# Performance work log

Measured on AMD Instinct MI355X. Metric: run time of the kernel, lower is better.

## Reference

```python
import jax, jax.numpy as jnp
import numpy as np

S, B, L = 64, 32, 64
VS, VT = 32000, 32000
D_EMB, H_ENC, H_DEC = 300, 512, 1024


def _lstm_cell(x, h, c, w_ih, w_hh, b):
    # PyTorch gate order: i, f, g, o
    g = x @ w_ih.T + h @ w_hh.T + b
    i, f, gg, o = jnp.split(g, 4, axis=1)
    c2 = jax.nn.sigmoid(f) * c + jax.nn.sigmoid(i) * jnp.tanh(gg)
    h2 = jax.nn.sigmoid(o) * jnp.tanh(c2)
    return h2, c2


def _lstm_dir(emb, w_ih, w_hh, b, reverse):
    h0 = jnp.zeros((emb.shape[1], H_ENC), emb.dtype)
    def step(carry, x):
        h, c = carry
        h, c = _lstm_cell(x, h, c, w_ih, w_hh, b)
        return (h, c), h
    (hT, cT), ys = jax.lax.scan(step, (h0, h0), emb, reverse=reverse)
    return ys, hT, cT


def setup_inputs() -> dict:
    key = jax.random.key(0)
    ks = jax.random.split(key, 20)
    r = lambda k, shape: (jax.random.normal(k, shape, jnp.float32) * 0.02)
    inp = {
        "eemb": r(ks[0], (VS, D_EMB)),
        "enc_w_ih_f": r(ks[1], (4 * H_ENC, D_EMB)),
        "enc_w_hh_f": r(ks[2], (4 * H_ENC, H_ENC)),
        "enc_b_f": r(ks[3], (4 * H_ENC,)),  # = b_ih + b_hh (summed, identical math)
        "enc_w_ih_b": r(ks[4], (4 * H_ENC, D_EMB)),
        "enc_w_hh_b": r(ks[5], (4 * H_ENC, H_ENC)),
        "enc_b_b": r(ks[6], (4 * H_ENC,)),
        "attn_wi": r(ks[7], (H_DEC, H_DEC)),
        "attn_wo": r(ks[8], (H_DEC, 2 * H_DEC)),
        "dec_w_ih": r(ks[9], (4 * H_DEC, H_DEC + D_EMB)),
        "dec_w_hh": r(ks[10], (4 * H_DEC, H_DEC)),
        "dec_b": r(ks[11], (4 * H_DEC,)),
        "demb": r(ks[12], (VT, D_EMB)),
        "gen_w": r(ks[13], (VT, H_DEC)),
        "gen_b": r(ks[14], (VT,)),
        "input_src_batch": jax.random.randint(ks[15], (S, B), 0, VS),
        "input_trg_batch": jax.random.randint(ks[16], (L, B), 0, VT),
    }
    return inp


def reference(eemb, enc_w_ih_f, enc_w_hh_f, enc_b_f, enc_w_ih_b, enc_w_hh_b,
              enc_b_b, attn_wi, attn_wo, dec_w_ih, dec_w_hh, dec_b, demb,
              gen_w, gen_b, input_src_batch, input_trg_batch):
    emb = eemb[input_src_batch]  # [S,B,300]
    out_f, hf, cf = _lstm_dir(emb, enc_w_ih_f, enc_w_hh_f, enc_b_f, False)
    out_b, hb, cb = _lstm_dir(emb, enc_w_ih_b, enc_w_hh_b, enc_b_b, True)
    enc_out = jnp.concatenate([out_f, out_b], axis=2)  # [S,B,1024]
    bsz = emb.shape[1]
    # permute(1,2,0).view(B,1024): interleave fwd/bwd features
    hidden = jnp.stack([hf, hb], 0).transpose(1, 2, 0).reshape(bsz, H_DEC)
    context = jnp.stack([cf, cb], 0).transpose(1, 2, 0).reshape(bsz, H_DEC)

    trg_emb = demb[input_trg_batch[:-1]]  # [L-1,B,300]

    def dec_step(carry, e):
        h, c = carry
        semi = h @ attn_wi.T  # [B,1024]
        scores = jax.nn.softmax(jnp.sum(enc_out * semi[None], axis=2), axis=0)  # [S,B]
        s_tilde = jnp.sum(scores[:, :, None] * enc_out, axis=0)  # [B,1024]
        c_t = jnp.tanh(jnp.concatenate([s_tilde, h], axis=1) @ attn_wo.T)
        x = jnp.concatenate([c_t, e], axis=1)  # [B,1324]
        h, c = _lstm_cell(x, h, c, dec_w_ih, dec_w_hh, dec_b)
        out = jax.nn.log_softmax(h @ gen_w.T + gen_b, axis=1)  # [B,VT]
        return (h, c), out

    _, ys = jax.lax.scan(dec_step, (hidden, context), trg_emb)  # [L-1,B,VT]
    output = jnp.concatenate([jnp.zeros((1,) + ys.shape[1:], ys.dtype), ys], axis=0)
    return output
```

## Files before the change

kernel.cpp:

```cpp
#include <hip/hip_runtime.h>

typedef __attribute__((ext_vector_type(8))) short short8;
typedef __attribute__((ext_vector_type(4))) float f32x4;
typedef unsigned short u16;
typedef unsigned int u32;

static __device__ __forceinline__ float sigf(float x){ return 1.0f/(1.0f+__expf(-x)); }
static __device__ __forceinline__ float ftanh(float x){
    float e = __expf(2.0f*x);
    return 1.0f - 2.0f/(e + 1.0f);
}

static __device__ __forceinline__ u16 f2b(float f){
    u32 u = __float_as_uint(f);
    u += 0x7FFFu + ((u>>16)&1u);
    return (u16)(u>>16);
}
static __device__ __forceinline__ float us2f(u16 s){ return __uint_as_float(((u32)s)<<16); }
static __device__ __forceinline__ float b2f_lo(u32 u){ return __uint_as_float(u<<16); }
static __device__ __forceinline__ float b2f_hi(u32 u){ return __uint_as_float(u & 0xffff0000u); }

static __device__ __forceinline__ void st_wt_u16(u16* p, u16 v) {
    asm volatile("global_store_short %0, %1, off sc1" :: "v"(p), "v"((u32)v) : "memory");
}
static __device__ __forceinline__ void st_wt_u32(u32* p, u32 v) {
    asm volatile("global_store_dword %0, %1, off sc1" :: "v"(p), "v"(v) : "memory");
}
static __device__ __forceinline__ u32 ld_cv(const u32* p){
    u32 v;
    asm volatile("global_load_dword %0, %1, off sc0 sc1\ns_waitcnt vmcnt(0)"
                 : "=v"(v) : "v"(p) : "memory");
    return v;
}

static __device__ __forceinline__ void hot_spin() {
    float x = 1.0f;
#pragma unroll
    for (int i = 0; i < 16; ++i) x = __builtin_fmaf(x, 1.0000001f, 1.0e-7f);
    asm volatile("" :: "v"(x));
}

static __device__ __forceinline__ void wait_publish(const u32* base, int n, u32 tgt, u32* rel) {
    if ((int)threadIdx.x < n) {
        const u32* p = base + (size_t)threadIdx.x*32;
        while (ld_cv(p) < tgt) hot_spin();
    }
    __syncthreads();
    if (threadIdx.x == 0) st_wt_u32(rel, tgt);
}
static __device__ __forceinline__ void wait_rel(const u32* rel, u32 tgt) {
    if (threadIdx.x == 0) {
        while (ld_cv(rel) < tgt) hot_spin();
    }
    __syncthreads();
}


__global__ __launch_bounds__(256) void k_zero(float* __restrict__ p, long n) {
    for (long i = (long)blockIdx.x*256 + threadIdx.x; i < n; i += (long)gridDim.x*256) p[i] = 0.0f;
}

__global__ __launch_bounds__(256) void k_wenc2(const float* __restrict__ whhf,
                                               const float* __restrict__ whhb,
                                               u16* __restrict__ dst) {
    long i = (long)blockIdx.x*256 + threadIdx.x;
    int half = (int)(i >> 20);
    int ii = (int)(i & 1048575);
    int n = ii >> 9, k = ii & 511;
    int j = n >> 2, q = n & 3;
    const float* w = half ? whhb : whhf;
    dst[i] = f2b(w[(size_t)(q*512 + j)*512 + k]);
}

__global__ __launch_bounds__(256) void k_xw(const float* __restrict__ table,
                                            const int* __restrict__ idx,
                                            const float* __restrict__ W,
                                            int wstride, int koff,
                                            const float* __restrict__ bias,
                                            u16* __restrict__ outU, int N,
                                            int jmask, int jshift) {
    __shared__ float Xs[32][300];
    int m0 = blockIdx.y * 32;
    int j0 = blockIdx.x * 64;
    for (int i = threadIdx.x; i < 32*300; i += 256) {
        int r = i/300, c = i - r*300;
        Xs[r][c] = table[(size_t)idx[m0+r]*300 + c];
    }
    __syncthreads();
    int tx = threadIdx.x & 63, ty = threadIdx.x >> 6;
    int jj = j0 + tx;
    const float* wr = W + (size_t)jj*wstride + koff;
    float acc[8] = {0,0,0,0,0,0,0,0};
    for (int k = 0; k < 300; ++k) {
        float w = wr[k];
#pragma unroll
        for (int mi = 0; mi < 8; ++mi) acc[mi] += Xs[ty*8+mi][k] * w;
    }
    float bv = bias[jj];
    int col = ((jj & jmask) << 2) | (jj >> jshift);
#pragma unroll
    for (int mi = 0; mi < 8; ++mi)
        outU[(size_t)(m0 + ty*8 + mi)*N + col] = f2b(acc[mi] + bv);
}

__global__ __launch_bounds__(512, 1) void k_enc(
    const u16* __restrict__ Xf, const u16* __restrict__ Xb,
    const u16* __restrict__ WencB,
    u16* __restrict__ encBX, float* __restrict__ cfin,
    u32* __restrict__ sentE, u32* __restrict__ relE,
    const float* __restrict__ awi, const float* __restrict__ awo,
    const float* __restrict__ dwih, const float* __restrict__ dwhh,
    const float* __restrict__ genw,
    u16* __restrict__ awiTB, u16* __restrict__ awoB,
    u16* __restrict__ WdecB, u16* __restrict__ genw_b)
{
    __shared__ float SH[2304];
    const int tid = threadIdx.x;
    const int bid = blockIdx.x;

    if (bid >= 64) {
        long wid = (long)(bid-64)*512 + tid;
        {
            const float4* s4 = (const float4*)genw;
            ushort4* d4 = (ushort4*)genw_b;
            for (long i = wid; i < 8192000L; i += 98304L) {
                float4 v = s4[i]; ushort4 u;
                u.x=f2b(v.x); u.y=f2b(v.y); u.z=f2b(v.z); u.w=f2b(v.w);
                d4[i]=u;
            }
        }
        for (long i = wid; i < 8388608L; i += 98304L) {
            int n=(int)(i>>11), k=(int)(i&2047);
            int j=n>>2, q=n&3;
            float v=(k<1024)? dwih[(size_t)(q*1024+j)*1324+k]
                            : dwhh[(size_t)(q*1024+j)*1024+(k-1024)];
            WdecB[i]=f2b(v);
        }
        for (long i = wid; i < 1048576L; i += 98304L) {
            int kcol=(int)(i>>10), n=(int)(i&1023);
            awiTB[i]=f2b(awi[(size_t)n*1024+kcol]);
        }
        {
            const float4* s4=(const float4*)awo;
            ushort4* d4=(ushort4*)awoB;
            for (long i = wid; i < 524288L; i += 98304L) {
                float4 v=s4[i]; ushort4 u;
                u.x=f2b(v.x); u.y=f2b(v.y); u.z=f2b(v.z); u.w=f2b(v.w);
                d4[i]=u;
            }
        }
        return;
    }

    const int wv = tid >> 6, lane = tid & 63;
    const int gwave = bid*8 + wv;
    const int lr = lane & 15, lk8 = (lane >> 4)*8;
    const int b_l = lane & 15, jjq = lane >> 4;
    const int g0 = bid & 48;
    u32* relg = relE + (size_t)(g0 >> 4)*32;

    const int dir = gwave >> 8;
    const int mt = (gwave >> 7) & 1;
    const int nt = gwave & 127;
    const int m0 = mt*16, n0 = nt*16;
    const u16* Bw = WencB + (size_t)dir*1048576 + (size_t)(n0+lr)*512 + lk8;
    const u16* Xd = dir ? Xb : Xf;
    float* T = SH + wv*272;
    const int bb = m0 + b_l;
    const int j = nt*4 + jjq;

    short8 bw[16];
#pragma unroll
    for (int i = 0; i < 16; ++i) bw[i] = *(const short8*)(Bw + i*32);

    float creg = 0.f;
    for (int t = 0; t < 64; ++t) {
        if (t > 0) {
            if (bid == g0) wait_publish(sentE + (size_t)g0*32, 16, (u32)t, relg);
            else           wait_rel(relg, (u32)t);
        }
        const int rslot = (t==0) ? 0 : (dir ? (65-t) : t);
        const u16* Ah = encBX + (size_t)rslot*32768 + (size_t)(m0+lr)*1024 + dir*512 + lk8;
        short8 av[16];
#pragma unroll
        for (int i = 0; i < 16; ++i) av[i] = *(const short8*)(Ah + i*32);
        f32x4 acc = {0.f,0.f,0.f,0.f};
#pragma unroll
        for (int i = 0; i < 16; ++i)
            acc = __builtin_amdgcn_mfma_f32_16x16x32_bf16(av[i], bw[i], acc, 0, 0, 0);
        {
            const int rb = (lane>>4)*4;
#pragma unroll
            for (int r = 0; r < 4; ++r) T[(rb+r)*17 + (lane&15)] = acc[r];
        }
        __builtin_amdgcn_sched_barrier(0);
        const int s = dir ? (63-t) : t;
        ushort4 xr = *(const ushort4*)(Xd + (size_t)(s*32+bb)*2048 + n0 + jjq*4);
        float gi = T[b_l*17 + jjq*4 + 0] + us2f(xr.x);
        float gf = T[b_l*17 + jjq*4 + 1] + us2f(xr.y);
        float gg = T[b_l*17 + jjq*4 + 2] + us2f(xr.z);
        float go = T[b_l*17 + jjq*4 + 3] + us2f(xr.w);
        float c2 = sigf(gf)*creg + sigf(gi)*ftanh(gg);
        float h2 = sigf(go)*ftanh(c2);
        creg = c2;
        st_wt_u16(encBX + (size_t)(s+1)*32768 + (size_t)bb*1024 + dir*512 + j, f2b(h2));
        __syncthreads();
        if (tid == 0) st_wt_u32(sentE + (size_t)bid*32, (u32)(t+1));
    }
    cfin[dir*16384 + bb*512 + j] = creg;
}

__global__ __launch_bounds__(256) void k_mid(const u16* __restrict__ encBX,
                                             const u16* __restrict__ awiTB,
                                             const u16* __restrict__ awoB,
                                             u16* __restrict__ encPB,
                                             u16* __restrict__ EOAb,
                                             u16* __restrict__ Hd) {
    if (blockIdx.x < 128) {
        int gt = blockIdx.x*256 + threadIdx.x;
        int b = gt >> 10, jj2 = gt & 1023;
        int d = jj2 & 1, k = jj2 >> 1;
        Hd[(size_t)b*1024 + jj2] = encBX[(size_t)(d ? 1 : 64)*32768 + (size_t)b*1024 + d*512 + k];
        Hd[(size_t)64*32768 + gt] = 0;
    }
    const int wv = threadIdx.x >> 6, lane = threadIdx.x & 63;
    const int lr = lane & 15, lk8 = (lane >> 4)*8;
    const u16* Abase = encBX + 32768;
#pragma unroll
    for (int ii = 0; ii < 4; ++ii) {
        int id = (blockIdx.x*4 + wv)*4 + ii;
        int eoa = id >> 13;
        int id2 = id & 8191;
        int mt2 = id2 >> 6, nt2 = id2 & 63;
        int m0 = mt2*16, n0 = nt2*16;
        const u16* Ar = Abase + (size_t)(m0+lr)*1024 + lk8;
        const u16* Br = eoa ? (awoB + (size_t)(n0+lr)*2048 + lk8)
                            : (awiTB + (size_t)(n0+lr)*1024 + lk8);
        f32x4 acc = {0.f,0.f,0.f,0.f};
#pragma unroll 8
        for (int i = 0; i < 32; ++i) {
            short8 av = *(const short8*)(Ar + i*32);
            short8 bv = *(const short8*)(Br + i*32);
            acc = __builtin_amdgcn_mfma_f32_16x16x32_bf16(av, bv, acc, 0, 0, 0);
        }
        int col = n0 + (lane&15);
        int rb = m0 + (lane>>4)*4;
#pragma unroll
        for (int r = 0; r < 4; ++r) {
            int row = rb + r;
            if (eoa) {
                int b = row & 31, s = row >> 5;
                EOAb[((size_t)b*64 + s)*1024 + col] = f2b(acc[r]);
            } else {
                encPB[(size_t)row*1024 + col] = f2b(acc[r]);
            }
        }
    }
}

__global__ __launch_bounds__(512, 1) void k_dec(
    const u16* __restrict__ Xe,
    const u16* __restrict__ awoB, const u16* __restrict__ WdecB,
    const u16* __restrict__ encPB, const u16* __restrict__ EOAb,
    u16* __restrict__ Hd, u16* __restrict__ PEOb, u16* __restrict__ hAb,
    const float* __restrict__ cfin,
    u32* __restrict__ sentA, u32* __restrict__ sentH,
    u32* __restrict__ relA, u32* __restrict__ relH)
{
    __shared__ float SH[2592];
    __shared__ u32 CT[16512];
    const int tid = threadIdx.x;
    const int bid = blockIdx.x;
    const int wv = tid >> 6, lane = tid & 63;
    const int lr = lane & 15, lk8 = (lane >> 4)*8;
    const int b_l = lane & 15, jjq = lane >> 4;

    const int mt4 = wv & 1, kq4 = wv >> 1;
    const int m0d = mt4*16;
    const int bbd = m0d + b_l;
    const int jd = bid*4 + jjq;
    float cdec = cfin[(jd&1)*16384 + bbd*512 + (jd>>1)];

    short8 wp[16];
#pragma unroll
    for (int i = 0; i < 16; ++i)
        wp[i] = *(const short8*)(WdecB + (size_t)(bid*16+lr)*2048 + kq4*512 + lk8 + i*32);

    const bool isHA = (bid >= 32 && bid < 96);
    const int nth = bid - 32;
    const int mth = wv & 1, kqh = wv >> 1;
    short8 wh[8];
    if (isHA) {
#pragma unroll
        for (int i = 0; i < 8; ++i)
            wh[i] = *(const short8*)(awoB + (size_t)(nth*16+lr)*2048 + 1024 + kqh*256 + lk8 + i*32);
    }

    for (int t = 0; t < 63; ++t) {
        if (bid < 96) {
            if (t > 0) {
                if (bid == 0) wait_publish(sentH, 256, (u32)t, relH);
                else          wait_rel(relH, (u32)t);
            }
            if (bid < 32) {
                const int b = bid;
                float* hsh = SH; float* red = SH + 1024; float* sc = SH + 1536;
                {
                    u32 u = ((const u32*)Hd)[(size_t)t*16384 + b*512 + tid];
                    hsh[2*tid]   = b2f_lo(u);
                    hsh[2*tid+1] = b2f_hi(u);
                }
                __syncthreads();
                {
                    int s = tid >> 3, p = tid & 7;
                    const uint4* ep = (const uint4*)(encPB + (size_t)(s*32+b)*1024 + p*128);
                    const float* hk = hsh + p*128;
                    float a0=0,a1=0,a2=0,a3=0;
#pragma unroll 4
                    for (int q8 = 0; q8 < 16; ++q8) {
                        uint4 u = ep[q8];
                        a0 += b2f_lo(u.x)*hk[q8*8+0] + b2f_hi(u.x)*hk[q8*8+1];
                        a1 += b2f_lo(u.y)*hk[q8*8+2] + b2f_hi(u.y)*hk[q8*8+3];
                        a2 += b2f_lo(u.z)*hk[q8*8+4] + b2f_hi(u.z)*hk[q8*8+5];
                        a3 += b2f_lo(u.w)*hk[q8*8+6] + b2f_hi(u.w)*hk[q8*8+7];
                    }
                    red[tid] = (a0+a1)+(a2+a3);
                }
                __syncthreads();
                if (tid < 64) {
                    float v = 0;
#pragma unroll
                    for (int pp = 0; pp < 8; ++pp) v += red[tid*8+pp];
                    float m = v;
                    for (int off = 32; off; off >>= 1) m = fmaxf(m, __shfl_xor(m, off));
                    float e = __expf(v - m);
                    float ss = e;
                    for (int off = 32; off; off >>= 1) ss += __shfl_xor(ss, off);
                    sc[tid] = e / ss;
                }
                __syncthreads();
                {
                    const u32* eo = (const u32*)EOAb + (size_t)b*32768 + tid;
                    float p0 = 0, p1 = 0;
#pragma unroll 8
                    for (int s = 0; s < 64; ++s) {
                        u32 u = eo[(size_t)s*512];
                        float w = sc[s];
                        p0 += w*b2f_lo(u); p1 += w*b2f_hi(u);
                    }
                    u32 pk = (u32)f2b(p0) | ((u32)f2b(p1) << 16);
                    st_wt_u32((u32*)PEOb + (size_t)t*16384 + b*512 + tid, pk);
                }
            } else {
                const u16* Ah = Hd + (size_t)t*32768 + (size_t)(mth*16+lr)*1024 + kqh*256 + lk8;
                short8 av[8];
#pragma unroll
                for (int i = 0; i < 8; ++i) av[i] = *(const short8*)(Ah + i*32);
                f32x4 acc = {0.f,0.f,0.f,0.f};
#pragma unroll
                for (int i = 0; i < 8; ++i)
                    acc = __builtin_amdgcn_mfma_f32_16x16x32_bf16(av[i], wh[i], acc, 0, 0, 0);
#pragma unroll
                for (int r = 0; r < 4; ++r) SH[wv*256 + lane*4 + r] = acc[r];
                __syncthreads();
                if (wv < 2) {
#pragma unroll
                    for (int r = 0; r < 4; ++r) {
                        float sum = SH[(wv+0)*256 + lane*4 + r] + SH[(wv+2)*256 + lane*4 + r]
                                  + SH[(wv+4)*256 + lane*4 + r] + SH[(wv+6)*256 + lane*4 + r];
                        int m = wv*16 + (lane>>4)*4 + r;
                        st_wt_u16(hAb + (size_t)t*32768 + (size_t)m*1024 + nth*16 + (lane&15),
                                  f2b(sum));
                    }
                }
            }
            __syncthreads();
            if (tid == 0) st_wt_u32(sentA + (size_t)bid*32, (u32)(t+1));
        }

        if (bid == 96) wait_publish(sentA, 96, (u32)(t+1), relA);
        else           wait_rel(relA, (u32)(t+1));
        {
            const u32* pe = (const u32*)PEOb + (size_t)t*16384;
            const u32* ha = (const u32*)hAb + (size_t)t*16384;
#pragma unroll
            for (int ii = 0; ii < 32; ++ii) {
                int idx = tid + ii*512;
                u32 up = pe[idx], uh = ha[idx];
                float c0 = ftanh(b2f_lo(up) + b2f_lo(uh));
                float c1 = ftanh(b2f_hi(up) + b2f_hi(uh));
                int b = idx >> 9, nu = idx & 511;
                CT[b*516 + nu] = (u32)f2b(c0) | ((u32)f2b(c1) << 16);
            }
            __syncthreads();

            short8 av[16];
            if (kq4 < 2) {
                const u32* ctrow = CT + (m0d+lr)*516 + kq4*256 + (lk8 >> 1);
#pragma unroll
                for (int i = 0; i < 16; ++i) av[i] = *(const short8*)(ctrow + i*16);
            } else {
                const u16* Ab = Hd + (size_t)t*32768 + (size_t)(m0d+lr)*1024 + (kq4-2)*512 + lk8;
#pragma unroll
                for (int i = 0; i < 16; ++i) av[i] = *(const short8*)(Ab + i*32);
            }
            f32x4 acc = {0.f,0.f,0.f,0.f};
#pragma unroll
            for (int i = 0; i < 16; ++i)
                acc = __builtin_amdgcn_mfma_f32_16x16x32_bf16(av[i], wp[i], acc, 0, 0, 0);
#pragma unroll
            for (int r = 0; r < 4; ++r) SH[wv*256 + lane*4 + r] = acc[r];
            __syncthreads();
            if (wv < 2) {
                float* T = SH + 2048 + wv*272;
#pragma unroll
                for (int r = 0; r < 4; ++r) {
                    float sum = SH[(wv+0)*256 + lane*4 + r] + SH[(wv+2)*256 + lane*4 + r]
                              + SH[(wv+4)*256 + lane*4 + r] + SH[(wv+6)*256 + lane*4 + r];
                    T[((lane>>4)*4 + r)*17 + (lane&15)] = sum;
                }
                __builtin_amdgcn_sched_barrier(0);
                ushort4 xr = *(const ushort4*)(Xe + (size_t)(t*32+bbd)*4096 + bid*16 + jjq*4);
                float gi = T[b_l*17 + jjq*4 + 0] + us2f(xr.x);
                float gf = T[b_l*17 + jjq*4 + 1] + us2f(xr.y);
                float gg = T[b_l*17 + jjq*4 + 2] + us2f(xr.z);
                float go = T[b_l*17 + jjq*4 + 3] + us2f(xr.w);
                float c2 = sigf(gf)*cdec + sigf(gi)*ftanh(gg);
                float h2 = sigf(go)*ftanh(c2);
                cdec = c2;
                st_wt_u16(Hd + (size_t)(t+1)*32768 + (size_t)bbd*1024 + jd, f2b(h2));
            }
            __syncthreads();
            if (tid == 0) st_wt_u32(sentH + (size_t)bid*32, (u32)(t+1));
        }
    }
}

__global__ __launch_bounds__(256, 1) void k_gemm_gen(const short* __restrict__ A,
                                                     const short* __restrict__ B,
                                                     const float* __restrict__ genb,
                                                     float* __restrict__ out) {
    int wave = threadIdx.x >> 6;
    int lane = threadIdx.x & 63;
    int tile = blockIdx.x * 4 + wave;
    int mt = tile & 15;
    int nt = tile >> 4;
    int m0 = mt*128, n0 = nt*64;
    int lr = lane & 15;
    int lk = (lane >> 4)*8;
    f32x4 acc[8][4] = {};
    for (int k0 = 0; k0 < 1024; k0 += 32) {
        short8 bfr[4];
#pragma unroll
        for (int ni = 0; ni < 4; ++ni)
            bfr[ni] = *(const short8*)(B + (long)(n0 + ni*16 + lr)*1024 + k0 + lk);
#pragma unroll
        for (int mi = 0; mi < 8; ++mi) {
            short8 a = *(const short8*)(A + (long)(m0 + mi*16 + lr)*1024 + k0 + lk);
#pragma unroll
            for (int ni = 0; ni < 4; ++ni)
                acc[mi][ni] = __builtin_amdgcn_mfma_f32_16x16x32_bf16(a, bfr[ni], acc[mi][ni], 0, 0, 0);
        }
    }
    int dcol = lane & 15;
    int drow = (lane >> 4)*4;
#pragma unroll
    for (int mi = 0; mi < 8; ++mi) {
        int mbase = m0 + mi*16 + drow;
#pragma unroll
        for (int ni = 0; ni < 4; ++ni) {
            int n = n0 + ni*16 + dcol;
            float bv = genb[n];
            f32x4 v = acc[mi][ni];
#pragma unroll
            for (int r = 0; r < 4; ++r) {
                int m = mbase + r;
                if (m < 2016) out[(long)(m + 32)*32000 + n] = v[r] + bv;
            }
        }
    }
}

__global__ __launch_bounds__(256) void k_lsm(float* __restrict__ out) {
    long row = 32 + blockIdx.x;
    float* p = out + row*32000L;
    float4* p4 = (float4*)p;
    int tid = threadIdx.x;
    __shared__ float sm[4];
    __shared__ float ss[4];
    float m = -1e30f;
    for (int i = tid; i < 8000; i += 256) {
        float4 v = p4[i];
        m = fmaxf(m, fmaxf(fmaxf(v.x, v.y), fmaxf(v.z, v.w)));
    }
    for (int off = 32; off; off >>= 1) m = fmaxf(m, __shfl_xor(m, off));
    if ((tid & 63) == 0) sm[tid >> 6] = m;
    __syncthreads();
    m = fmaxf(fmaxf(sm[0], sm[1]), fmaxf(sm[2], sm[3]));
    float s = 0;
    for (int i = tid; i < 8000; i += 256) {
        float4 v = p4[i];
        s += __expf(v.x - m) + __expf(v.y - m) + __expf(v.z - m) + __expf(v.w - m);
    }
    for (int off = 32; off; off >>= 1) s += __shfl_xor(s, off);
    if ((tid & 63) == 0) ss[tid >> 6] = s;
    __syncthreads();
    s = ss[0] + ss[1] + ss[2] + ss[3];
    float lse = m + __logf(s);
    for (int i = tid; i < 8000; i += 256) {
        float4 v = p4[i];
        v.x -= lse; v.y -= lse; v.z -= lse; v.w -= lse;
        p4[i] = v;
    }
}


extern "C" void kernel_launch(void* const* d_in, const int* in_sizes, int n_in,
                              void* d_out, int out_size, void* d_ws, size_t ws_size,
                              hipStream_t stream) {
    const float* eemb  = (const float*)d_in[0];
    const float* ewihf = (const float*)d_in[1];
    const float* ewhhf = (const float*)d_in[2];
    const float* ebf   = (const float*)d_in[3];
    const float* ewihb = (const float*)d_in[4];
    const float* ewhhb = (const float*)d_in[5];
    const float* ebb   = (const float*)d_in[6];
    const float* awi   = (const float*)d_in[7];
    const float* awo   = (const float*)d_in[8];
    const float* dwih  = (const float*)d_in[9];
    const float* dwhh  = (const float*)d_in[10];
    const float* db    = (const float*)d_in[11];
    const float* demb  = (const float*)d_in[12];
    const float* genw  = (const float*)d_in[13];
    const float* genb  = (const float*)d_in[14];
    const int* srci    = (const int*)d_in[15];
    const int* trgi    = (const int*)d_in[16];
    float* out = (float*)d_out;

    float* F = (float*)d_ws;
    u32* S       = (u32*)F;
    u32* sentE   = S;
    u32* sentA   = S + 2048;
    u32* sentH   = S + 5120;
    u32* relE    = S + 13312;
    u32* relA    = S + 13440;
    u32* relH    = S + 13472;
    float* cfin  = F + 16384;
    u16*   U     = (u16*)(F + 49152);

    u16* Xf_    = U;
    u16* Xb_    = U + 4194304u;
    u16* Xe_    = U + 8388608u;
    u16* WencB  = U + 16646144u;
    u16* awiTB  = U + 18743296u;
    u16* awoB   = U + 19791872u;
    u16* WdecB  = U + 21889024u;
    u16* genw_b = U + 30277632u;
    u16* encBX  = U + 63045632u;
    u16* Hd     = U + 65175552u;
    u16* PEOb   = U + 67305472u;
    u16* hAb    = U + 69369856u;
    u16* encPB  = U + 71434240u;
    u16* EOAb   = U + 73531392u;

    k_zero<<<64, 256, 0, stream>>>(F, 16384);
    k_zero<<<64, 256, 0, stream>>>((float*)encBX, 16384);
    k_zero<<<2048, 256, 0, stream>>>(out, 1024000L);

    k_xw<<<dim3(32, 64), 256, 0, stream>>>(eemb, srci, ewihf, 300, 0, ebf, Xf_, 2048, 511, 9);
    k_xw<<<dim3(32, 64), 256, 0, stream>>>(eemb, srci, ewihb, 300, 0, ebb, Xb_, 2048, 511, 9);
    k_xw<<<dim3(64, 63), 256, 0, stream>>>(demb, trgi, dwih, 1324, 1024, db, Xe_, 4096, 1023, 10);

    k_wenc2<<<8192, 256, 0, stream>>>(ewhhf, ewhhb, WencB);

    k_enc<<<256, 512, 0, stream>>>(Xf_, Xb_, WencB, encBX, cfin, sentE, relE,
                                   awi, awo, dwih, dwhh, genw,
                                   awiTB, awoB, WdecB, genw_b);
    k_mid<<<1024, 256, 0, stream>>>(encBX, awiTB, awoB, encPB, EOAb, Hd);

    k_dec<<<256, 512, 0, stream>>>(Xe_, awoB, WdecB, encPB, EOAb,
                                   Hd, PEOb, hAb, cfin,
                                   sentA, sentH, relA, relH);

    k_gemm_gen<<<2000, 256, 0, stream>>>((const short*)(Hd + 32768u), (const short*)genw_b, genb, out);
    k_lsm<<<2016, 256, 0, stream>>>(out);
}
```

Baseline: 2.633 ms.

## Overlap generator GEMM with decoder recurrence inside persistent decode kernel

Halves the number of blocks doing the decoder LSTM update, so each block now handles two batch halves (32 gate columns), which frees blocks 128-255. Those freed blocks compute the vocabulary projection GEMM in chunks of 256 rows as soon as the corresponding hidden states are published. The aim is to hide the large generator GEMM behind the latency-bound sequential decode and drop a separate kernel launch. In exchange, the decoder blocks do twice the MFMA work per step, the shared-memory footprint grows, and the GEMM blocks compete with the recurrence for bandwidth and caches.

```diff
diff --git a/kernel.cpp b/kernel.cpp
--- a/kernel.cpp
+++ b/kernel.cpp
@@ -264,10 +264,11 @@
     const u16* __restrict__ encPB, const u16* __restrict__ EOAb,
     u16* __restrict__ Hd, u16* __restrict__ PEOb, u16* __restrict__ hAb,
     const float* __restrict__ cfin,
+    const u16* __restrict__ genw_b, const float* __restrict__ genb, float* __restrict__ out,
     u32* __restrict__ sentA, u32* __restrict__ sentH,
     u32* __restrict__ relA, u32* __restrict__ relH)
 {
-    __shared__ float SH[2592];
+    __shared__ float SH[5184];
     __shared__ u32 CT[16512];
     const int tid = threadIdx.x;
     const int bid = blockIdx.x;
@@ -275,16 +276,64 @@
     const int lr = lane & 15, lk8 = (lane >> 4)*8;
     const int b_l = lane & 15, jjq = lane >> 4;
 
-    const int mt4 = wv & 1, kq4 = wv >> 1;
-    const int m0d = mt4*16;
-    const int bbd = m0d + b_l;
-    const int jd = bid*4 + jjq;
-    float cdec = cfin[(jd&1)*16384 + bbd*512 + (jd>>1)];
+    if (bid >= 128) {
+        const int gw = (bid - 128)*8 + wv;
+        const u16* A = Hd + 32768;
+        for (int c = 0; c < 8; ++c) {
+            u32 need = (c == 7) ? 63u : (u32)(8*c + 8);
+            wait_rel(relH, need);
+            int tile = gw;
+            if (tile < 1000) {
+                int m0 = c*256 + (tile & 1)*128;
+                int n0 = (tile >> 1)*64;
+                f32x4 acc[8][4] = {};
+                for (int k0 = 0; k0 < 1024; k0 += 32) {
+                    short8 bfr[4];
+#pragma unroll
+                    for (int ni = 0; ni < 4; ++ni)
+                        bfr[ni] = *(const short8*)(genw_b + (size_t)(n0 + ni*16 + lr)*1024 + k0 + lk8);
+#pragma unroll
+                    for (int mi = 0; mi < 8; ++mi) {
+                        short8 a = *(const short8*)(A + (size_t)(m0 + mi*16 + lr)*1024 + k0 + lk8);
+#pragma unroll
+                        for (int ni = 0; ni < 4; ++ni)
+                            acc[mi][ni] = __builtin_amdgcn_mfma_f32_16x16x32_bf16(a, bfr[ni], acc[mi][ni], 0, 0, 0);
+                    }
+                }
+                int dcol = lane & 15;
+                int drow = (lane >> 4)*4;
+#pragma unroll
+                for (int mi = 0; mi < 8; ++mi) {
+                    int mbase = m0 + mi*16 + drow;
+#pragma unroll
+                    for (int ni = 0; ni < 4; ++ni) {
+                        int n = n0 + ni*16 + dcol;
+                        float bv = genb[n];
+                        f32x4 v = acc[mi][ni];
+#pragma unroll
+                        for (int r = 0; r < 4; ++r) {
+                            int m = mbase + r;
+                            if (m < 2016) out[(size_t)(m + 32)*32000 + n] = v[r] + bv;
+                        }
+                    }
+                }
+            }
+        }
+        return;
+    }
+
+    const int ntB = wv & 1, kqB = wv >> 1;
+    const int jdB = bid*8 + ntB*4 + jjq;
+    float cdec0 = 0.f, cdec1 = 0.f;
+    if (wv < 2) {
+        cdec0 = cfin[(jdB&1)*16384 + (b_l)*512 + (jdB>>1)];
+        cdec1 = cfin[(jdB&1)*16384 + (16+b_l)*512 + (jdB>>1)];
+    }
 
     short8 wp[16];
 #pragma unroll
     for (int i = 0; i < 16; ++i)
-        wp[i] = *(const short8*)(WdecB + (size_t)(bid*16+lr)*2048 + kq4*512 + lk8 + i*32);
+        wp[i] = *(const short8*)(WdecB + (size_t)(bid*32 + ntB*16 + lr)*2048 + kqB*512 + lk8 + i*32);
 
     const bool isHA = (bid >= 32 && bid < 96);
     const int nth = bid - 32;
@@ -297,11 +346,9 @@
     }
 
     for (int t = 0; t < 63; ++t) {
+        if (t > 0 && bid == 97) wait_publish(sentH, 128, (u32)t, relH);
         if (bid < 96) {
-            if (t > 0) {
-                if (bid == 0) wait_publish(sentH, 256, (u32)t, relH);
-                else          wait_rel(relH, (u32)t);
-            }
+            if (t > 0) wait_rel(relH, (u32)t);
             if (bid < 32) {
                 const int b = bid;
                 float* hsh = SH; float* red = SH + 1024; float* sc = SH + 1536;
@@ -394,91 +441,77 @@
             }
             __syncthreads();
 
-            short8 av[16];
-            if (kq4 < 2) {
-                const u32* ctrow = CT + (m0d+lr)*516 + kq4*256 + (lk8 >> 1);
-#pragma unroll
-                for (int i = 0; i < 16; ++i) av[i] = *(const short8*)(ctrow + i*16);
+            f32x4 a0 = {0.f,0.f,0.f,0.f}, a1 = {0.f,0.f,0.f,0.f};
+            if (kqB < 2) {
+                const u32* c0p = CT + (lr)*516 + kqB*256 + (lk8 >> 1);
+                const u32* c1p = CT + (16+lr)*516 + kqB*256 + (lk8 >> 1);
+#pragma unroll
+                for (int i = 0; i < 16; ++i) {
+                    short8 v0 = *(const short8*)(c0p + i*16);
+                    short8 v1 = *(const short8*)(c1p + i*16);
+                    a0 = __builtin_amdgcn_mfma_f32_16x16x32_bf16(v0, wp[i], a0, 0, 0, 0);
+                    a1 = __builtin_amdgcn_mfma_f32_16x16x32_bf16(v1, wp[i], a1, 0, 0, 0);
+                }
             } else {
-                const u16* Ab = Hd + (size_t)t*32768 + (size_t)(m0d+lr)*1024 + (kq4-2)*512 + lk8;
-#pragma unroll
-                for (int i = 0; i < 16; ++i) av[i] = *(const short8*)(Ab + i*32);
-            }
-            f32x4 acc = {0.f,0.f,0.f,0.f};
-#pragma unroll
-            for (int i = 0; i < 16; ++i)
-                acc = __builtin_amdgcn_mfma_f32_16x16x32_bf16(av[i], wp[i], acc, 0, 0, 0);
-#pragma unroll
-            for (int r = 0; r < 4; ++r) SH[wv*256 + lane*4 + r] = acc[r];
+                const u16* h0p = Hd + (size_t)t*32768 + (size_t)(lr)*1024 + (kqB-2)*512 + lk8;
+                const u16* h1p = Hd + (size_t)t*32768 + (size_t)(16+lr)*1024 + (kqB-2)*512 + lk8;
+#pragma unroll
+                for (int i = 0; i < 16; ++i) {
+                    short8 v0 = *(const short8*)(h0p + i*32);
+                    short8 v1 = *(const short8*)(h1p + i*32);
+                    a0 = __builtin_amdgcn_mfma_f32_16x16x32_bf16(v0, wp[i], a0, 0, 0, 0);
+                    a1 = __builtin_amdgcn_mfma_f32_16x16x32_bf16(v1, wp[i], a1, 0, 0, 0);
+                }
+            }
+#pragma unroll
+            for (int r = 0; r < 4; ++r) {
+                SH[wv*512 + lane*4 + r] = a0[r];
+                SH[wv*512 + 256 + lane*4 + r] = a1[r];
+            }
             __syncthreads();
             if (wv < 2) {
-                float* T = SH + 2048 + wv*272;
+                const int nt = wv;
+                float* T0 = SH + 4096 + (wv*2+0)*272;
+                float* T1 = SH + 4096 + (wv*2+1)*272;
 #pragma unroll
                 for (int r = 0; r < 4; ++r) {
-                    float sum = SH[(wv+0)*256 + lane*4 + r] + SH[(wv+2)*256 + lane*4 + r]
-                              + SH[(wv+4)*256 + lane*4 + r] + SH[(wv+6)*256 + lane*4 + r];
-                    T[((lane>>4)*4 + r)*17 + (lane&15)] = sum;
+                    float s0 = SH[(nt+0)*512 + lane*4 + r] + SH[(nt+2)*512 + lane*4 + r]
+                             + SH[(nt+4)*512 + lane*4 + r] + SH[(nt+6)*512 + lane*4 + r];
+                    float s1 = SH[(nt+0)*512 + 256 + lane*4 + r] + SH[(nt+2)*512 + 256 + lane*4 + r]
+                             + SH[(nt+4)*512 + 256 + lane*4 + r] + SH[(nt+6)*512 + 256 + lane*4 + r];
+                    int rr = ((lane>>4)*4 + r)*17 + (lane&15);
+                    T0[rr] = s0;
+                    T1[rr] = s1;
                 }
                 __builtin_amdgcn_sched_barrier(0);
-                ushort4 xr = *(const ushort4*)(Xe + (size_t)(t*32+bbd)*4096 + bid*16 + jjq*4);
-                float gi = T[b_l*17 + jjq*4 + 0] + us2f(xr.x);
-                float gf = T[b_l*17 + jjq*4 + 1] + us2f(xr.y);
-                float gg = T[b_l*17 + jjq*4 + 2] + us2f(xr.z);
-                float go = T[b_l*17 + jjq*4 + 3] + us2f(xr.w);
-                float c2 = sigf(gf)*cdec + sigf(gi)*ftanh(gg);
-                float h2 = sigf(go)*ftanh(c2);
-                cdec = c2;
-                st_wt_u16(Hd + (size_t)(t+1)*32768 + (size_t)bbd*1024 + jd, f2b(h2));
+                {
+                    ushort4 xr = *(const ushort4*)(Xe + (size_t)(t*32 + b_l)*4096 + jdB*4);
+                    float gi = T0[b_l*17 + jjq*4 + 0] + us2f(xr.x);
+                    float gf = T0[b_l*17 + jjq*4 + 1] + us2f(xr.y);
+                    float gg = T0[b_l*17 + jjq*4 + 2] + us2f(xr.z);
+                    float go = T0[b_l*17 + jjq*4 + 3] + us2f(xr.w);
+                    float c2 = sigf(gf)*cdec0 + sigf(gi)*ftanh(gg);
+                    float h2 = sigf(go)*ftanh(c2);
+                    cdec0 = c2;
+                    st_wt_u16(Hd + (size_t)(t+1)*32768 + (size_t)b_l*1024 + jdB, f2b(h2));
+                }
+                {
+                    ushort4 xr = *(const ushort4*)(Xe + (size_t)(t*32 + 16 + b_l)*4096 + jdB*4);
+                    float gi = T1[b_l*17 + jjq*4 + 0] + us2f(xr.x);
+                    float gf = T1[b_l*17 + jjq*4 + 1] + us2f(xr.y);
+                    float gg = T1[b_l*17 + jjq*4 + 2] + us2f(xr.z);
+                    float go = T1[b_l*17 + jjq*4 + 3] + us2f(xr.w);
+                    float c2 = sigf(gf)*cdec1 + sigf(gi)*ftanh(gg);
+                    float h2 = sigf(go)*ftanh(c2);
+                    cdec1 = c2;
+                    st_wt_u16(Hd + (size_t)(t+1)*32768 + (size_t)(16+b_l)*1024 + jdB, f2b(h2));
+                }
             }
             __syncthreads();
             if (tid == 0) st_wt_u32(sentH + (size_t)bid*32, (u32)(t+1));
         }
     }
-}
-
-__global__ __launch_bounds__(256, 1) void k_gemm_gen(const short* __restrict__ A,
-                                                     const short* __restrict__ B,
-                                                     const float* __restrict__ genb,
-                                                     float* __restrict__ out) {
-    int wave = threadIdx.x >> 6;
-    int lane = threadIdx.x & 63;
-    int tile = blockIdx.x * 4 + wave;
-    int mt = tile & 15;
-    int nt = tile >> 4;
-    int m0 = mt*128, n0 = nt*64;
-    int lr = lane & 15;
-    int lk = (lane >> 4)*8;
-    f32x4 acc[8][4] = {};
-    for (int k0 = 0; k0 < 1024; k0 += 32) {
-        short8 bfr[4];
-#pragma unroll
-        for (int ni = 0; ni < 4; ++ni)
-            bfr[ni] = *(const short8*)(B + (long)(n0 + ni*16 + lr)*1024 + k0 + lk);
-#pragma unroll
-        for (int mi = 0; mi < 8; ++mi) {
-            short8 a = *(const short8*)(A + (long)(m0 + mi*16 + lr)*1024 + k0 + lk);
-#pragma unroll
-            for (int ni = 0; ni < 4; ++ni)
-                acc[mi][ni] = __builtin_amdgcn_mfma_f32_16x16x32_bf16(a, bfr[ni], acc[mi][ni], 0, 0, 0);
-        }
-    }
-    int dcol = lane & 15;
-    int drow = (lane >> 4)*4;
-#pragma unroll
-    for (int mi = 0; mi < 8; ++mi) {
-        int mbase = m0 + mi*16 + drow;
-#pragma unroll
-        for (int ni = 0; ni < 4; ++ni) {
-            int n = n0 + ni*16 + dcol;
-            float bv = genb[n];
-            f32x4 v = acc[mi][ni];
-#pragma unroll
-            for (int r = 0; r < 4; ++r) {
-                int m = mbase + r;
-                if (m < 2016) out[(long)(m + 32)*32000 + n] = v[r] + bv;
-            }
-        }
-    }
+    if (bid == 97) wait_publish(sentH, 128, 63u, relH);
 }
 
 __global__ __launch_bounds__(256) void k_lsm(float* __restrict__ out) {
@@ -580,8 +613,8 @@
 
     k_dec<<<256, 512, 0, stream>>>(Xe_, awoB, WdecB, encPB, EOAb,
                                    Hd, PEOb, hAb, cfin,
+                                   genw_b, genb, out,
                                    sentA, sentH, relA, relH);
 
-    k_gemm_gen<<<2000, 256, 0, stream>>>((const short*)(Hd + 32768u), (const short*)genw_b, genb, out);
     k_lsm<<<2016, 256, 0, stream>>>(out);
 }
```

After: 2.480 ms. 5.8% less time.
